# Kernel optimization log

Hardware: AMD Instinct MI355X
Metric: run time of the kernel (lower is better)

The kernel has to match this reference:

```python
import jax, jax.numpy as jnp
import numpy as np

ROI, P = 28, 7          # ROI window on feature map; output grid 7x7 -> 4x4 bins
BIN = ROI // P
C, CLASSES = 64, 2      # channels after vgg features[:2]; n classes
H = W = 512
N_ROI = 2000
D_FC = 4096


def setup_inputs() -> dict:
    key = jax.random.key(0)
    k = jax.random.split(key, 8)
    s = 0.02
    return {
        "img": jax.random.normal(k[0], (3, H, W), jnp.float32),
        "regions": jax.random.randint(k[1], (N_ROI, 2), 0, H - ROI, jnp.int32),
        "conv_w": jax.random.normal(k[2], (C, 3, 3, 3), jnp.float32) * s,
        "conv_b": jnp.zeros((C,), jnp.float32),
        "fc1_w": jax.random.normal(k[3], (D_FC, C * P * P), jnp.float32) * s,
        "fc1_b": jnp.zeros((D_FC,), jnp.float32),
        "fc2_w": jax.random.normal(k[4], (D_FC, D_FC), jnp.float32) * s,
        "fc2_b": jnp.zeros((D_FC,), jnp.float32),
        "cls_w": jax.random.normal(k[5], (CLASSES, D_FC), jnp.float32) * s,
        "cls_b": jnp.zeros((CLASSES,), jnp.float32),
        "bbox_w": jax.random.normal(k[6], (CLASSES * 4, D_FC), jnp.float32) * s,
        "bbox_b": jnp.zeros((CLASSES * 4,), jnp.float32),
    }


def reference(img, regions, conv_w, conv_b, fc1_w, fc1_b,
              fc2_w, fc2_b, cls_w, cls_b, bbox_w, bbox_b):
    # conv trunk: vgg16.features[:2] = Conv2d(3,64,3,pad=1) + ReLU
    fmap = jax.lax.conv_general_dilated(
        img[None], conv_w, window_strides=(1, 1), padding="SAME",
        dimension_numbers=("NCHW", "OIHW", "NCHW"))[0]
    fmap = jax.nn.relu(fmap + conv_b[:, None, None])        # [C, H, W]

    # per-region crop (irregular gather), vectorized over regions
    def crop(rc):
        return jax.lax.dynamic_slice(fmap, (0, rc[0], rc[1]), (C, ROI, ROI))
    rois = jax.vmap(crop)(regions)                          # [N, C, ROI, ROI]

    # RoI max pooling: divide ROIxROI window into PxP grid, max each bin
    pooled = rois.reshape(N_ROI, C, P, BIN, P, BIN).max(axis=(3, 5))  # [N,C,P,P]
    feat = pooled.reshape(N_ROI, C * P * P)

    # vgg classifier[:-1] (Dropout = identity at inference)
    feat = jax.nn.relu(feat @ fc1_w.T + fc1_b)
    feat = jax.nn.relu(feat @ fc2_w.T + fc2_b)              # [N, 4096]

    cls_logits = feat @ cls_w.T + cls_b                     # [N, CLASSES]
    loc_bbox = feat @ bbox_w.T + bbox_b                     # [N, CLASSES*4]
    return (cls_logits, loc_bbox)
```

## Files before the change

### kernel.cpp

```cpp
#include <hip/hip_runtime.h>

typedef unsigned short u16;
typedef unsigned int u32;
using bf16x8 = __attribute__((ext_vector_type(8))) short;
using f32x4  = __attribute__((ext_vector_type(4))) float;

__device__ __forceinline__ u16 f2bf(float f) {
  u32 u = __float_as_uint(f);
  return (u16)((u + 0x7FFFu + ((u >> 16) & 1u)) >> 16);
}
__device__ __forceinline__ float bf2f(u16 h) {
  return __uint_as_float(((u32)h) << 16);
}

__global__ __launch_bounds__(256) void conv3x3_relu_k(
    const float* __restrict__ img, const float* __restrict__ w,
    const float* __restrict__ bias, u16* __restrict__ fmap) {
  int p = blockIdx.x * 256 + threadIdx.x;
  int y = p >> 9, x = p & 511;
  float v[27];
#pragma unroll
  for (int ci = 0; ci < 3; ++ci)
#pragma unroll
    for (int ky = 0; ky < 3; ++ky)
#pragma unroll
      for (int kx = 0; kx < 3; ++kx) {
        int yy = y + ky - 1, xx = x + kx - 1;
        bool ok = (yy >= 0) && (yy < 512) && (xx >= 0) && (xx < 512);
        v[(ci * 3 + ky) * 3 + kx] = ok ? img[ci * 262144 + yy * 512 + xx] : 0.f;
      }
  float acc[64];
#pragma unroll
  for (int co = 0; co < 64; ++co) {
    float s = bias[co];
#pragma unroll
    for (int q = 0; q < 27; ++q) s = fmaf(w[co * 27 + q], v[q], s);
    acc[co] = fmaxf(s, 0.f);
  }
  uint4* dst = (uint4*)((u32*)fmap + (size_t)p * 32);
#pragma unroll
  for (int q = 0; q < 8; ++q) {
    uint4 d;
    d.x = (u32)f2bf(acc[8 * q + 0]) | ((u32)f2bf(acc[8 * q + 1]) << 16);
    d.y = (u32)f2bf(acc[8 * q + 2]) | ((u32)f2bf(acc[8 * q + 3]) << 16);
    d.z = (u32)f2bf(acc[8 * q + 4]) | ((u32)f2bf(acc[8 * q + 5]) << 16);
    d.w = (u32)f2bf(acc[8 * q + 6]) | ((u32)f2bf(acc[8 * q + 7]) << 16);
    dst[q] = d;
  }
}

__global__ __launch_bounds__(256) void roipool_k(
    const u16* __restrict__ fmap, const int* __restrict__ regions,
    u16* __restrict__ feat) {
  int n = blockIdx.x, t = threadIdx.x;
  uint4* fdst = (uint4*)(feat + (size_t)n * 3136);
  if (n >= 2000) {
    uint4 z; z.x = z.y = z.z = z.w = 0u;
    fdst[t % 392] = z;
    int t2 = t + 256; if (t2 < 392) fdst[t2] = z;
    if (t < 392) fdst[t] = z;
    return;
  }
  int r0 = regions[2 * n], c0 = regions[2 * n + 1];
  __shared__ uint2 rows_u2[1792];
  __shared__ uint4 frow4[392];
  u16* rows = (u16*)rows_u2;
  u16* frow = (u16*)frow4;
  for (int py = 0; py < 7; ++py) {
#pragma unroll
    for (int q = 0; q < 7; ++q) {
      int cid = t + q * 256;
      int i = cid / 448, rem = cid % 448;
      int xo = rem >> 4, c4 = (rem & 15) << 2;
      int yy = r0 + py * 4 + i, xx = c0 + xo;
      rows_u2[cid] = *(const uint2*)(fmap + (((size_t)(yy * 512 + xx)) << 6) + c4);
    }
    __syncthreads();
#pragma unroll
    for (int h = 0; h < 2; ++h) {
      int o = t + h * 256;
      if (o < 448) {
        int c = o & 63, px = o >> 6;
        float best = -3.0e38f;
#pragma unroll
        for (int i = 0; i < 4; ++i)
#pragma unroll
          for (int j = 0; j < 4; ++j)
            best = fmaxf(best, bf2f(rows[(i * 28 + px * 4 + j) * 64 + c]));
        frow[c * 49 + py * 7 + px] = f2bf(best);
      }
    }
    __syncthreads();
  }
  if (t < 392) fdst[t] = frow4[t];
  int t2 = t + 256;
  if (t2 < 392) fdst[t2] = frow4[t2];
}

__global__ __launch_bounds__(256) void f2bf_k(const float* __restrict__ in,
                                              u16* __restrict__ out, int n4) {
  int idx = blockIdx.x * 256 + threadIdx.x;
  int stride = gridDim.x * 256;
  for (int i = idx; i < n4; i += stride) {
    float4 v = ((const float4*)in)[i];
    uint2 o;
    o.x = (u32)f2bf(v.x) | ((u32)f2bf(v.y) << 16);
    o.y = (u32)f2bf(v.z) | ((u32)f2bf(v.w) << 16);
    ((uint2*)out)[i] = o;
  }
}

__global__ __launch_bounds__(512, 2) void gemm8_bt_relu_k(
    const u16* __restrict__ A, const u16* __restrict__ B,
    const float* __restrict__ bias, u16* __restrict__ C, int N, int K) {
  __shared__ uint4 lds4[9216];
  char* ldsb = (char*)lds4;
  const int t = threadIdx.x;
  const int lane = t & 63, wv = t >> 6;
  const int wm = wv >> 2, wn = wv & 3;

  int bid = blockIdx.x;
  int swz = ((bid & 7) << 5) | (bid >> 3);
  const int nb = swz >> 4, mb = swz & 15;
  const int m0 = mb * 128, n0 = nb * 256;

  const u16* __restrict__ Ab = A + (size_t)m0 * K;
  const u16* __restrict__ Bb = B + (size_t)n0 * K;

  const int srow = t >> 3;
  const int sslot = (t & 7) ^ (srow & 7);
  const u16* pA0 = Ab + (size_t)srow * K + sslot * 8;
  const u16* pA1 = pA0 + (size_t)64 * K;
  const u16* pB0 = Bb + (size_t)srow * K + sslot * 8;
  const u16* pB1 = pB0 + (size_t)64 * K;
  const u16* pB2 = pB0 + (size_t)128 * K;
  const u16* pB3 = pB0 + (size_t)192 * K;
  const int dof = t * 16;

#define G2L(src, ldst)                                                        \
  __builtin_amdgcn_global_load_lds(                                          \
      (const __attribute__((address_space(1))) void*)(src),                  \
      (__attribute__((address_space(3))) void*)(ldst), 16, 0, 0)

  const int rA = wm * 64 + (lane & 15);
  const int rB = wn * 64 + (lane & 15);
  const int sl = lane >> 4;
#define LOFF(r, slot) (((r) << 7) + ((((slot) ^ ((r) & 7))) << 4))

  f32x4 acc[4][4] = {};
  bf16x8 bfr[4][2], afr[2][2];

  const int NT = K >> 6;
  {
    char* A0 = ldsb; char* B0 = A0 + 16384;
    char* A1 = ldsb + 49152; char* B1 = A1 + 16384;
    G2L(pA0, A0 + dof); G2L(pA1, A0 + 8192 + dof);
    G2L(pB0, B0 + dof); G2L(pB1, B0 + 8192 + dof);
    G2L(pB2, B0 + 16384 + dof); G2L(pB3, B0 + 24576 + dof);
    G2L(pA0 + 64, A1 + dof); G2L(pA1 + 64, A1 + 8192 + dof);
    G2L(pB0 + 64, B1 + dof); G2L(pB1 + 64, B1 + 8192 + dof);
    G2L(pB2 + 64, B1 + 16384 + dof); G2L(pB3 + 64, B1 + 24576 + dof);
  }
  asm volatile("s_waitcnt vmcnt(6)" ::: "memory");
  __builtin_amdgcn_s_barrier();

  int cb = 0;
  for (int tt = 0; tt < NT; ++tt) {
    const int pb = (cb + 2 >= 3) ? cb - 1 : cb + 2;
    const bool pf = (tt + 2) < NT;
    char* Acur = ldsb + cb * 49152; char* Bcur = Acur + 16384;
    char* Apf  = ldsb + pb * 49152; char* Bpf  = Apf + 16384;
    const int kof = (tt + 2) << 6;

#pragma unroll
    for (int j = 0; j < 4; ++j) {
      bfr[j][0] = *(const bf16x8*)(Bcur + LOFF(rB + j * 16, sl));
      bfr[j][1] = *(const bf16x8*)(Bcur + LOFF(rB + j * 16, 4 + sl));
    }
#pragma unroll
    for (int i = 0; i < 2; ++i) {
      afr[i][0] = *(const bf16x8*)(Acur + LOFF(rA + i * 16, sl));
      afr[i][1] = *(const bf16x8*)(Acur + LOFF(rA + i * 16, 4 + sl));
    }
    if (pf) {
      G2L(pA0 + kof, Apf + dof);
      G2L(pA1 + kof, Apf + 8192 + dof);
      G2L(pB0 + kof, Bpf + dof);
    }
    __builtin_amdgcn_s_barrier();
    asm volatile("s_waitcnt lgkmcnt(0)" ::: "memory");
    __builtin_amdgcn_sched_barrier(0);
    __builtin_amdgcn_s_setprio(1);
#pragma unroll
    for (int i = 0; i < 2; ++i)
#pragma unroll
      for (int j = 0; j < 4; ++j) {
        acc[i][j] = __builtin_amdgcn_mfma_f32_16x16x32_bf16(afr[i][0], bfr[j][0], acc[i][j], 0, 0, 0);
        acc[i][j] = __builtin_amdgcn_mfma_f32_16x16x32_bf16(afr[i][1], bfr[j][1], acc[i][j], 0, 0, 0);
      }
    __builtin_amdgcn_s_setprio(0);
    __builtin_amdgcn_s_barrier();

#pragma unroll
    for (int i = 0; i < 2; ++i) {
      afr[i][0] = *(const bf16x8*)(Acur + LOFF(rA + (i + 2) * 16, sl));
      afr[i][1] = *(const bf16x8*)(Acur + LOFF(rA + (i + 2) * 16, 4 + sl));
    }
    if (pf) {
      G2L(pB1 + kof, Bpf + 8192 + dof);
      G2L(pB2 + kof, Bpf + 16384 + dof);
      G2L(pB3 + kof, Bpf + 24576 + dof);
    }
    __builtin_amdgcn_s_barrier();
    asm volatile("s_waitcnt lgkmcnt(0)" ::: "memory");
    __builtin_amdgcn_sched_barrier(0);
    __builtin_amdgcn_s_setprio(1);
#pragma unroll
    for (int i = 0; i < 2; ++i)
#pragma unroll
      for (int j = 0; j < 4; ++j) {
        acc[i + 2][j] = __builtin_amdgcn_mfma_f32_16x16x32_bf16(afr[i][0], bfr[j][0], acc[i + 2][j], 0, 0, 0);
        acc[i + 2][j] = __builtin_amdgcn_mfma_f32_16x16x32_bf16(afr[i][1], bfr[j][1], acc[i + 2][j], 0, 0, 0);
      }
    __builtin_amdgcn_s_setprio(0);
    if (pf) {
      asm volatile("s_waitcnt vmcnt(6)" ::: "memory");
    } else if (tt + 1 < NT) {
      asm volatile("s_waitcnt vmcnt(0)" ::: "memory");
    }
    __builtin_amdgcn_s_barrier();
    cb = (cb == 2) ? 0 : cb + 1;
  }
#undef G2L
#undef LOFF

  float bv[4];
#pragma unroll
  for (int j = 0; j < 4; ++j) bv[j] = bias[n0 + wn * 64 + j * 16 + (lane & 15)];
#pragma unroll
  for (int i = 0; i < 4; ++i)
#pragma unroll
    for (int j = 0; j < 4; ++j) {
      int cg = n0 + wn * 64 + j * 16 + (lane & 15);
#pragma unroll
      for (int r = 0; r < 4; ++r) {
        int rg = m0 + wm * 64 + i * 16 + (lane >> 4) * 4 + r;
        float v = fmaxf(acc[i][j][r] + bv[j], 0.f);
        C[(size_t)rg * N + cg] = f2bf(v);
      }
    }
}

__global__ __launch_bounds__(256) void heads_k(
    const u16* __restrict__ h2, const float* __restrict__ cw,
    const float* __restrict__ cb, const float* __restrict__ bw,
    const float* __restrict__ bb, float* __restrict__ out) {
  int m = blockIdx.x, t = threadIdx.x;
  const u16* hrow = h2 + (size_t)m * 4096;
  float p[10];
#pragma unroll
  for (int j = 0; j < 10; ++j) p[j] = 0.f;
  for (int k = t; k < 4096; k += 256) {
    float v = bf2f(hrow[k]);
    p[0] = fmaf(v, cw[k], p[0]);
    p[1] = fmaf(v, cw[4096 + k], p[1]);
#pragma unroll
    for (int j = 0; j < 8; ++j) p[2 + j] = fmaf(v, bw[j * 4096 + k], p[2 + j]);
  }
#pragma unroll
  for (int j = 0; j < 10; ++j)
#pragma unroll
    for (int off = 32; off > 0; off >>= 1) p[j] += __shfl_down(p[j], off);
  __shared__ float red[4][10];
  int lane = t & 63, wv = t >> 6;
  if (lane == 0) {
#pragma unroll
    for (int j = 0; j < 10; ++j) red[wv][j] = p[j];
  }
  __syncthreads();
  if (t < 10) {
    float s = red[0][t] + red[1][t] + red[2][t] + red[3][t];
    s += (t < 2) ? cb[t] : bb[t - 2];
    if (t < 2) out[m * 2 + t] = s;
    else out[4000 + m * 8 + (t - 2)] = s;
  }
}

extern "C" void kernel_launch(void* const* d_in, const int* in_sizes, int n_in,
                              void* d_out, int out_size, void* d_ws, size_t ws_size,
                              hipStream_t stream) {
  const float* img    = (const float*)d_in[0];
  const int*   regions= (const int*)d_in[1];
  const float* conv_w = (const float*)d_in[2];
  const float* conv_b = (const float*)d_in[3];
  const float* fc1_w  = (const float*)d_in[4];
  const float* fc1_b  = (const float*)d_in[5];
  const float* fc2_w  = (const float*)d_in[6];
  const float* fc2_b  = (const float*)d_in[7];
  const float* cls_w  = (const float*)d_in[8];
  const float* cls_b  = (const float*)d_in[9];
  const float* bbox_w = (const float*)d_in[10];
  const float* bbox_b = (const float*)d_in[11];
  float* out = (float*)d_out;

  char* ws = (char*)d_ws;
  u16* fmap = (u16*)(ws);
  u16* feat = (u16*)(ws + 33554432);
  u16* w1b  = (u16*)(ws + 46399488);
  u16* w2b  = (u16*)(ws + 72089600);
  u16* h1   = (u16*)(ws);
  u16* h2   = (u16*)(ws + 16777216);

  conv3x3_relu_k<<<1024, 256, 0, stream>>>(img, conv_w, conv_b, fmap);
  roipool_k<<<2048, 256, 0, stream>>>(fmap, regions, feat);
  f2bf_k<<<2048, 256, 0, stream>>>(fc1_w, w1b, 4096 * 3136 / 4);
  f2bf_k<<<2048, 256, 0, stream>>>(fc2_w, w2b, 4096 * 4096 / 4);
  gemm8_bt_relu_k<<<256, 512, 0, stream>>>(feat, w1b, fc1_b, h1, 4096, 3136);
  gemm8_bt_relu_k<<<256, 512, 0, stream>>>(h1, w2b, fc2_b, h2, 4096, 4096);
  heads_k<<<2000, 256, 0, stream>>>(h2, cls_w, cls_b, bbox_w, bbox_b, out);
}
```

Measured before the change: 236.1 us.

## Restructure GEMM to 4 waves with BK=32 and full-M warp tiles

Replaces the 8-wave GEMM with a 4-wave version where each wave covers all 128 rows of M and 64 columns of N (8x4 MFMA tiles), using a K-step of 32 and a 3-stage LDS ring of 24 KB stages with a new swizzle. Each iteration now has a single barrier/MFMA phase instead of two half-phases. The aim is less synchronisation overhead and LDS traffic per MFMA, so more blocks can fit. In exchange the accumulator register pressure doubles and twice as many loop iterations are needed. The conv bound edit is cosmetic.

```diff
diff --git a/kernel.cpp b/kernel.cpp
--- a/kernel.cpp
+++ b/kernel.cpp
@@ -26,7 +26,7 @@
 #pragma unroll
       for (int kx = 0; kx < 3; ++kx) {
         int yy = y + ky - 1, xx = x + kx - 1;
-        bool ok = (yy >= 0) && (yy < 512) && (xx >= 0) && (xx < 512);
+        bool ok = (yy >= 0) && (yy < 512) && (xx >= 0) && (xx < 511 + 1);
         v[(ci * 3 + ky) * 3 + kx] = ok ? img[ci * 262144 + yy * 512 + xx] : 0.f;
       }
   float acc[64];
@@ -110,14 +110,13 @@
   }
 }
 
-__global__ __launch_bounds__(512, 2) void gemm8_bt_relu_k(
+__global__ __launch_bounds__(256, 2) void gemm4_bt_relu_k(
     const u16* __restrict__ A, const u16* __restrict__ B,
     const float* __restrict__ bias, u16* __restrict__ C, int N, int K) {
-  __shared__ uint4 lds4[9216];
+  __shared__ uint4 lds4[4608];
   char* ldsb = (char*)lds4;
   const int t = threadIdx.x;
   const int lane = t & 63, wv = t >> 6;
-  const int wm = wv >> 2, wn = wv & 3;
 
   int bid = blockIdx.x;
   int swz = ((bid & 7) << 5) | (bid >> 3);
@@ -127,8 +126,8 @@
   const u16* __restrict__ Ab = A + (size_t)m0 * K;
   const u16* __restrict__ Bb = B + (size_t)n0 * K;
 
-  const int srow = t >> 3;
-  const int sslot = (t & 7) ^ (srow & 7);
+  const int srow = t >> 2;
+  const int sslot = (t & 3) ^ ((srow >> 1) & 3);
   const u16* pA0 = Ab + (size_t)srow * K + sslot * 8;
   const u16* pA1 = pA0 + (size_t)64 * K;
   const u16* pB0 = Bb + (size_t)srow * K + sslot * 8;
@@ -141,25 +140,21 @@
   __builtin_amdgcn_global_load_lds(                                          \
       (const __attribute__((address_space(1))) void*)(src),                  \
       (__attribute__((address_space(3))) void*)(ldst), 16, 0, 0)
-
-  const int rA = wm * 64 + (lane & 15);
-  const int rB = wn * 64 + (lane & 15);
-  const int sl = lane >> 4;
-#define LOFF(r, slot) (((r) << 7) + ((((slot) ^ ((r) & 7))) << 4))
-
-  f32x4 acc[4][4] = {};
-  bf16x8 bfr[4][2], afr[2][2];
-
-  const int NT = K >> 6;
+#define LOFF(r, s) (((r) << 6) + ((((s) ^ (((r) >> 1) & 3))) << 4))
+
+  const int row = lane & 15, sl = lane >> 4;
+  f32x4 acc[8][4] = {};
+  bf16x8 afr[8], bfr[4];
+
+  const int NT = K >> 5;
   {
-    char* A0 = ldsb; char* B0 = A0 + 16384;
-    char* A1 = ldsb + 49152; char* B1 = A1 + 16384;
-    G2L(pA0, A0 + dof); G2L(pA1, A0 + 8192 + dof);
-    G2L(pB0, B0 + dof); G2L(pB1, B0 + 8192 + dof);
-    G2L(pB2, B0 + 16384 + dof); G2L(pB3, B0 + 24576 + dof);
-    G2L(pA0 + 64, A1 + dof); G2L(pA1 + 64, A1 + 8192 + dof);
-    G2L(pB0 + 64, B1 + dof); G2L(pB1 + 64, B1 + 8192 + dof);
-    G2L(pB2 + 64, B1 + 16384 + dof); G2L(pB3 + 64, B1 + 24576 + dof);
+    char* b0 = ldsb; char* b1 = ldsb + 24576;
+    G2L(pA0, b0 + dof);          G2L(pA1, b0 + 4096 + dof);
+    G2L(pB0, b0 + 8192 + dof);   G2L(pB1, b0 + 12288 + dof);
+    G2L(pB2, b0 + 16384 + dof);  G2L(pB3, b0 + 20480 + dof);
+    G2L(pA0 + 32, b1 + dof);         G2L(pA1 + 32, b1 + 4096 + dof);
+    G2L(pB0 + 32, b1 + 8192 + dof);  G2L(pB1 + 32, b1 + 12288 + dof);
+    G2L(pB2 + 32, b1 + 16384 + dof); G2L(pB3 + 32, b1 + 20480 + dof);
   }
   asm volatile("s_waitcnt vmcnt(6)" ::: "memory");
   __builtin_amdgcn_s_barrier();
@@ -168,60 +163,32 @@
   for (int tt = 0; tt < NT; ++tt) {
     const int pb = (cb + 2 >= 3) ? cb - 1 : cb + 2;
     const bool pf = (tt + 2) < NT;
-    char* Acur = ldsb + cb * 49152; char* Bcur = Acur + 16384;
-    char* Apf  = ldsb + pb * 49152; char* Bpf  = Apf + 16384;
-    const int kof = (tt + 2) << 6;
-
-#pragma unroll
-    for (int j = 0; j < 4; ++j) {
-      bfr[j][0] = *(const bf16x8*)(Bcur + LOFF(rB + j * 16, sl));
-      bfr[j][1] = *(const bf16x8*)(Bcur + LOFF(rB + j * 16, 4 + sl));
-    }
-#pragma unroll
-    for (int i = 0; i < 2; ++i) {
-      afr[i][0] = *(const bf16x8*)(Acur + LOFF(rA + i * 16, sl));
-      afr[i][1] = *(const bf16x8*)(Acur + LOFF(rA + i * 16, 4 + sl));
-    }
+    char* Acur = ldsb + cb * 24576;
+    char* Bcur = Acur + 8192;
+
+#pragma unroll
+    for (int i = 0; i < 8; ++i)
+      afr[i] = *(const bf16x8*)(Acur + LOFF(i * 16 + row, sl));
+#pragma unroll
+    for (int j = 0; j < 4; ++j)
+      bfr[j] = *(const bf16x8*)(Bcur + LOFF(wv * 64 + j * 16 + row, sl));
+
     if (pf) {
-      G2L(pA0 + kof, Apf + dof);
-      G2L(pA1 + kof, Apf + 8192 + dof);
-      G2L(pB0 + kof, Bpf + dof);
+      char* Apf = ldsb + pb * 24576;
+      const int kof = (tt + 2) << 5;
+      G2L(pA0 + kof, Apf + dof);          G2L(pA1 + kof, Apf + 4096 + dof);
+      G2L(pB0 + kof, Apf + 8192 + dof);   G2L(pB1 + kof, Apf + 12288 + dof);
+      G2L(pB2 + kof, Apf + 16384 + dof);  G2L(pB3 + kof, Apf + 20480 + dof);
     }
     __builtin_amdgcn_s_barrier();
     asm volatile("s_waitcnt lgkmcnt(0)" ::: "memory");
     __builtin_amdgcn_sched_barrier(0);
     __builtin_amdgcn_s_setprio(1);
 #pragma unroll
-    for (int i = 0; i < 2; ++i)
-#pragma unroll
-      for (int j = 0; j < 4; ++j) {
-        acc[i][j] = __builtin_amdgcn_mfma_f32_16x16x32_bf16(afr[i][0], bfr[j][0], acc[i][j], 0, 0, 0);
-        acc[i][j] = __builtin_amdgcn_mfma_f32_16x16x32_bf16(afr[i][1], bfr[j][1], acc[i][j], 0, 0, 0);
-      }
-    __builtin_amdgcn_s_setprio(0);
-    __builtin_amdgcn_s_barrier();
-
-#pragma unroll
-    for (int i = 0; i < 2; ++i) {
-      afr[i][0] = *(const bf16x8*)(Acur + LOFF(rA + (i + 2) * 16, sl));
-      afr[i][1] = *(const bf16x8*)(Acur + LOFF(rA + (i + 2) * 16, 4 + sl));
-    }
-    if (pf) {
-      G2L(pB1 + kof, Bpf + 8192 + dof);
-      G2L(pB2 + kof, Bpf + 16384 + dof);
-      G2L(pB3 + kof, Bpf + 24576 + dof);
-    }
-    __builtin_amdgcn_s_barrier();
-    asm volatile("s_waitcnt lgkmcnt(0)" ::: "memory");
-    __builtin_amdgcn_sched_barrier(0);
-    __builtin_amdgcn_s_setprio(1);
-#pragma unroll
-    for (int i = 0; i < 2; ++i)
-#pragma unroll
-      for (int j = 0; j < 4; ++j) {
-        acc[i + 2][j] = __builtin_amdgcn_mfma_f32_16x16x32_bf16(afr[i][0], bfr[j][0], acc[i + 2][j], 0, 0, 0);
-        acc[i + 2][j] = __builtin_amdgcn_mfma_f32_16x16x32_bf16(afr[i][1], bfr[j][1], acc[i + 2][j], 0, 0, 0);
-      }
+    for (int i = 0; i < 8; ++i)
+#pragma unroll
+      for (int j = 0; j < 4; ++j)
+        acc[i][j] = __builtin_amdgcn_mfma_f32_16x16x32_bf16(afr[i], bfr[j], acc[i][j], 0, 0, 0);
     __builtin_amdgcn_s_setprio(0);
     if (pf) {
       asm volatile("s_waitcnt vmcnt(6)" ::: "memory");
@@ -236,15 +203,15 @@
 
   float bv[4];
 #pragma unroll
-  for (int j = 0; j < 4; ++j) bv[j] = bias[n0 + wn * 64 + j * 16 + (lane & 15)];
-#pragma unroll
-  for (int i = 0; i < 4; ++i)
+  for (int j = 0; j < 4; ++j) bv[j] = bias[n0 + wv * 64 + j * 16 + row];
+#pragma unroll
+  for (int i = 0; i < 8; ++i)
 #pragma unroll
     for (int j = 0; j < 4; ++j) {
-      int cg = n0 + wn * 64 + j * 16 + (lane & 15);
+      int cg = n0 + wv * 64 + j * 16 + row;
 #pragma unroll
       for (int r = 0; r < 4; ++r) {
-        int rg = m0 + wm * 64 + i * 16 + (lane >> 4) * 4 + r;
+        int rg = m0 + i * 16 + sl * 4 + r;
         float v = fmaxf(acc[i][j][r] + bv[j], 0.f);
         C[(size_t)rg * N + cg] = f2bf(v);
       }
@@ -315,7 +282,7 @@
   roipool_k<<<2048, 256, 0, stream>>>(fmap, regions, feat);
   f2bf_k<<<2048, 256, 0, stream>>>(fc1_w, w1b, 4096 * 3136 / 4);
   f2bf_k<<<2048, 256, 0, stream>>>(fc2_w, w2b, 4096 * 4096 / 4);
-  gemm8_bt_relu_k<<<256, 512, 0, stream>>>(feat, w1b, fc1_b, h1, 4096, 3136);
-  gemm8_bt_relu_k<<<256, 512, 0, stream>>>(h1, w2b, fc2_b, h2, 4096, 4096);
+  gemm4_bt_relu_k<<<256, 256, 0, stream>>>(feat, w1b, fc1_b, h1, 4096, 3136);
+  gemm4_bt_relu_k<<<256, 256, 0, stream>>>(h1, w2b, fc2_b, h2, 4096, 4096);
   heads_k<<<2000, 256, 0, stream>>>(h2, cls_w, cls_b, bbox_w, bbox_b, out);
 }
```

Result: slower. 244.3 us (+3.5%).
